# Kernel tuning notes

Measured on AMD Instinct MI355X. Metric: run time of the kernel, lower is better.

## Reference

```python
import jax, jax.numpy as jnp
import numpy as np

B, C, T = 4, 512, 4096


def setup_inputs() -> dict:
    key = jax.random.key(0)
    ks = jax.random.split(key, 9)
    s = 1.0 / np.sqrt(C)
    return {
        "x": jax.random.normal(ks[0], (B, C, T), jnp.float32),
        "Wq": jax.random.normal(ks[1], (C, C), jnp.float32) * s,
        "bq": jax.random.normal(ks[2], (C,), jnp.float32) * 0.01,
        "Wk": jax.random.normal(ks[3], (C, C), jnp.float32) * s,
        "bk": jax.random.normal(ks[4], (C,), jnp.float32) * 0.01,
        "Wv": jax.random.normal(ks[5], (C, C), jnp.float32) * s,
        "bv": jax.random.normal(ks[6], (C,), jnp.float32) * 0.01,
        "Wp": jax.random.normal(ks[7], (C, C), jnp.float32) * s,
        "bp": jax.random.normal(ks[8], (C,), jnp.float32) * 0.01,
    }


def reference(x, Wq, bq, Wk, bk, Wv, bv, Wp, bp):
    # x: [B, C, T]; kernel-size-1 causal convs == pointwise linears over channels.
    b, c, t = x.shape
    q = jnp.einsum('oc,bct->bto', Wq, x) + bq  # [B, T, C]
    k = jnp.einsum('oc,bct->bto', Wk, x) + bk
    v = jnp.einsum('oc,bct->bto', Wv, x) + bv
    scale = jnp.asarray(c, x.dtype) ** -0.5
    w = jnp.einsum('btc,bsc->bts', q, k) * scale  # [B, T, T]
    mask = jnp.tril(jnp.ones((t, t), bool))        # causal: query t attends s<=t
    w = jnp.where(mask, w, -jnp.inf)
    w = jax.nn.softmax(w, axis=-1)
    h = jnp.einsum('bts,bsc->btc', w, v)           # [B, T, C]
    out = jnp.einsum('oc,btc->bot', Wp, h) + bp[None, :, None]  # [B, C, T]
    return x + out
```

## Files before the change

kernel.cpp:

```cpp
#include <hip/hip_runtime.h>

#define NB 4
#define NC 512
#define NT 4096
#define NTILE 528

typedef __attribute__((ext_vector_type(4))) float f32x4;
typedef __attribute__((ext_vector_type(8))) short short8;

typedef const __attribute__((address_space(1))) unsigned int* gp1_t;
typedef __attribute__((address_space(3))) unsigned int* lp3_t;

__device__ __forceinline__ void gload16(const short* g, short* l) {
  __builtin_amdgcn_global_load_lds((gp1_t)g, (lp3_t)l, 16, 0, 0);
}

#define BARRIER() asm volatile("s_barrier" ::: "memory")
#define WAITVM0() asm volatile("s_waitcnt vmcnt(0)" ::: "memory")
#define WAITVM4() asm volatile("s_waitcnt vmcnt(4)" ::: "memory")
#define WAITVM8() asm volatile("s_waitcnt vmcnt(8)" ::: "memory")

__device__ __forceinline__ short f2bf(float f) {
  union { float f; unsigned u; } v; v.f = f;
  unsigned r = v.u + 0x7fffu + ((v.u >> 16) & 1u);
  return (short)(r >> 16);
}
__device__ __forceinline__ float bf2f(short s) {
  union { unsigned u; float f; } v; v.u = ((unsigned)(unsigned short)s) << 16;
  return v.f;
}

__device__ __forceinline__ void gemm_tile(const short* __restrict__ A, int lda,
                                          const short* __restrict__ Bg, int ldb,
                                          int m0, int n0, int ksteps,
                                          f32x4 (&acc)[4][4], short* lds) {
  const int tid  = threadIdx.x;
  const int lane = tid & 63;
  const int wv   = tid >> 6;
  const int wm = (wv >> 1) * 64;
  const int wn = (wv & 1) * 64;
  const int srow = wv * 16 + (lane >> 2);
  const int scol = (lane & 3) * 8;
  const int fm  = lane & 15;
  const int fko = (lane >> 4) * 8;

  const short* Ap0 = A  + (size_t)(m0 + srow) * lda + scol;
  const short* Ap1 = Ap0 + (size_t)64 * lda;
  const short* Bp0 = Bg + (size_t)(n0 + srow) * ldb + scol;
  const short* Bp1 = Bp0 + (size_t)64 * ldb;

  auto issue = [&](int kt) {
    short* base = lds + (kt % 3) * 8192;
    const int k0 = kt * 32;
    gload16(Ap0 + k0, base + wv * 512);
    gload16(Ap1 + k0, base + 2048 + wv * 512);
    gload16(Bp0 + k0, base + 4096 + wv * 512);
    gload16(Bp1 + k0, base + 6144 + wv * 512);
  };

  issue(0);
  if (ksteps > 1) issue(1);
  for (int kt = 0; kt < ksteps; ++kt) {
    const short* As = lds + (kt % 3) * 8192;
    const short* Bs = As + 4096;
    if (kt) BARRIER();
    if (kt + 2 < ksteps)      { issue(kt + 2); WAITVM8(); }
    else if (kt + 1 < ksteps) { WAITVM4(); }
    else                      { WAITVM0(); }
    BARRIER();
    short8 af[4], bfr[4];
#pragma unroll
    for (int i = 0; i < 4; ++i)
      af[i] = *(const short8*)(As + (wm + i * 16 + fm) * 32 + fko);
#pragma unroll
    for (int j = 0; j < 4; ++j)
      bfr[j] = *(const short8*)(Bs + (wn + j * 16 + fm) * 32 + fko);
#pragma unroll
    for (int i = 0; i < 4; ++i)
#pragma unroll
      for (int j = 0; j < 4; ++j)
        acc[i][j] = __builtin_amdgcn_mfma_f32_16x16x32_bf16(af[i], bfr[j], acc[i][j], 0, 0, 0);
  }
}

#define ACC_INIT                                  \
  f32x4 acc[4][4];                                \
  {                                               \
    const f32x4 z = {0.f, 0.f, 0.f, 0.f};         \
    for (int i = 0; i < 4; ++i)                   \
      for (int j = 0; j < 4; ++j) acc[i][j] = z;  \
  }

#define EPI_IDX                                   \
  const int lane = threadIdx.x & 63;              \
  const int wave = threadIdx.x >> 6;              \
  const int wm = (wave >> 1) * 64;                \
  const int wn = (wave & 1) * 64;

#define GEMM_LDS __shared__ short lds[24576];

__device__ __forceinline__ void xcd_rowchunk(int x, int nrows, int& row, int& chunk) {
  const int xcd  = x & 7;
  const int slot = x >> 3;
  row   = nrows - 1 - (xcd + 8 * (slot >> 2));
  chunk = slot & 3;
}

__global__ __launch_bounds__(256) void k_transpose(const float* __restrict__ x,
                                                   short* __restrict__ xT) {
  __shared__ float tile[32][33];
  const int b  = blockIdx.z;
  const int t0 = blockIdx.x * 32;
  const int c0 = blockIdx.y * 32;
  const int tx = threadIdx.x & 31;
  const int ty = threadIdx.x >> 5;
  const float* xp = x + ((size_t)b * NC + c0) * NT + t0;
#pragma unroll
  for (int i = 0; i < 32; i += 8)
    tile[ty + i][tx] = xp[(size_t)(ty + i) * NT + tx];
  __syncthreads();
  short* op = xT + ((size_t)b * NT + t0) * NC + c0;
#pragma unroll
  for (int i = 0; i < 32; i += 8)
    op[(size_t)(ty + i) * NC + tx] = f2bf(tile[tx][ty + i]);
}

__global__ __launch_bounds__(256) void k_wcvt(const float* __restrict__ s0, const float* __restrict__ s1,
                                              const float* __restrict__ s2, const float* __restrict__ s3,
                                              short* __restrict__ d0, short* __restrict__ d1,
                                              short* __restrict__ d2, short* __restrict__ d3) {
  const float* s; short* d;
  switch (blockIdx.y) {
    case 0: s = s0; d = d0; break;
    case 1: s = s1; d = d1; break;
    case 2: s = s2; d = d2; break;
    default: s = s3; d = d3; break;
  }
  const int i = (blockIdx.x * 256 + threadIdx.x) * 4;
  const float4 v = *(const float4*)(s + i);
  short4 o;
  o.x = f2bf(v.x); o.y = f2bf(v.y); o.z = f2bf(v.z); o.w = f2bf(v.w);
  *(short4*)(d + i) = o;
}

__global__ __launch_bounds__(256, 3) void k_qkv(const short* __restrict__ xT,
                                                const short* __restrict__ Wq,
                                                const float* __restrict__ bq,
                                                const short* __restrict__ Wk,
                                                const float* __restrict__ bk,
                                                const short* __restrict__ Wv,
                                                const float* __restrict__ bv,
                                                short* __restrict__ Q,
                                                short* __restrict__ K,
                                                short* __restrict__ VT) {
  GEMM_LDS;
  const int b = blockIdx.z;
  const int y = blockIdx.y;
  int row, chunk;
  xcd_rowchunk((int)blockIdx.x, NT / 128, row, chunk);
  const short* Xb = xT + (size_t)b * NT * NC;
  ACC_INIT;
  if (y < 2) {
    const short* W = (y == 0) ? Wq : Wk;
    const float* bias = (y == 0) ? bq : bk;
    short* O = ((y == 0) ? Q : K) + (size_t)b * NT * NC;
    const int m0 = row * 128;
    const int n0 = chunk * 128;
    gemm_tile(Xb, NC, W, NC, m0, n0, NC / 32, acc, lds);
    EPI_IDX;
#pragma unroll
    for (int j = 0; j < 4; ++j) {
      const int n = n0 + wn + j * 16 + (lane & 15);
      const float bv_ = bias[n];
#pragma unroll
      for (int i = 0; i < 4; ++i) {
        const int mb = m0 + wm + i * 16 + ((lane >> 4) * 4);
#pragma unroll
        for (int r = 0; r < 4; ++r)
          O[(size_t)(mb + r) * NC + n] = f2bf(acc[i][j][r] + bv_);
      }
    }
  } else {
    const int n0 = row * 128;
    const int m0 = chunk * 128;
    gemm_tile(Wv, NC, Xb, NC, m0, n0, NC / 32, acc, lds);
    EPI_IDX;
    short* O = VT + (size_t)b * NC * NT;
#pragma unroll
    for (int j = 0; j < 4; ++j) {
      const int n = n0 + wn + j * 16 + (lane & 15);
#pragma unroll
      for (int i = 0; i < 4; ++i) {
        const int mb = m0 + wm + i * 16 + ((lane >> 4) * 4);
#pragma unroll
        for (int r = 0; r < 4; ++r)
          O[(size_t)(mb + r) * NT + n] = f2bf(acc[i][j][r] + bv[mb + r]);
      }
    }
  }
}

__global__ __launch_bounds__(256, 3) void k_scores(const short* __restrict__ Q,
                                                   const short* __restrict__ K,
                                                   short* __restrict__ P,
                                                   float* __restrict__ Lrow) {
  const int p = (((int)blockIdx.x & 7) * 66) + ((int)blockIdx.x >> 3);
  int bm = 0, bn = 0;
  {
    int base = 0;
    for (int sr = 0; sr < 4; ++sr) {
      bool done = false;
      for (int sc = 0; sc <= sr; ++sc) {
        const int sz = (sc == sr) ? 36 : 64;
        if (p < base + sz) {
          const int q = p - base;
          int i, j;
          if (sc == sr) {
            i = 0;
            while ((i + 1) * (i + 2) / 2 <= q) ++i;
            j = q - i * (i + 1) / 2;
          } else { i = q >> 3; j = q & 7; }
          bm = sr * 8 + i; bn = sc * 8 + j;
          done = true; break;
        }
        base += sz;
      }
      if (done) break;
    }
  }
  GEMM_LDS;
  const int b  = blockIdx.z;
  const int m0 = bm * 128;
  const int n0 = bn * 128;
  ACC_INIT;
  gemm_tile(Q + (size_t)b * NT * NC, NC, K + (size_t)b * NT * NC, NC,
            m0, n0, NC / 32, acc, lds);
  EPI_IDX;
  const float scale = 0.04419417382415922f;
  const int idx = bm * (bm + 1) / 2 + bn;
  short* Tp = P + ((size_t)b * NTILE + (size_t)idx) * 16384;
  float* Lp = Lrow + (size_t)b * NT;
  float psum[4][4];
#pragma unroll
  for (int i = 0; i < 4; ++i)
#pragma unroll
    for (int r = 0; r < 4; ++r) psum[i][r] = 0.f;

  if (bn < bm) {
#pragma unroll
    for (int j = 0; j < 4; ++j) {
      const int ln = wn + j * 16 + (lane & 15);
#pragma unroll
      for (int i = 0; i < 4; ++i) {
        const int lmb = wm + i * 16 + ((lane >> 4) * 4);
#pragma unroll
        for (int r = 0; r < 4; ++r) {
          const short pb = f2bf(__expf(acc[i][j][r] * scale));
          Tp[(lmb + r) * 128 + ln] = pb;
          psum[i][r] += bf2f(pb);
        }
      }
    }
  } else {
#pragma unroll
    for (int j = 0; j < 4; ++j) {
      const int ln = wn + j * 16 + (lane & 15);
      const int n  = n0 + ln;
#pragma unroll
      for (int i = 0; i < 4; ++i) {
        const int lmb = wm + i * 16 + ((lane >> 4) * 4);
#pragma unroll
        for (int r = 0; r < 4; ++r) {
          const int m = m0 + lmb + r;
          float pr = 0.f;
          short pb = 0;
          if (n <= m) {
            pb = f2bf(__expf(acc[i][j][r] * scale));
            pr = bf2f(pb);
          }
          Tp[(lmb + r) * 128 + ln] = pb;
          psum[i][r] += pr;
        }
      }
    }
  }
#pragma unroll
  for (int i = 0; i < 4; ++i)
#pragma unroll
    for (int r = 0; r < 4; ++r) {
      float v = psum[i][r];
      v += __shfl_xor(v, 1);
      v += __shfl_xor(v, 2);
      v += __shfl_xor(v, 4);
      v += __shfl_xor(v, 8);
      if ((lane & 15) == 0) {
        const int m = m0 + wm + i * 16 + ((lane >> 4) * 4) + r;
        atomicAdd(&Lp[m], v);
      }
    }
}

__global__ __launch_bounds__(256, 3) void k_pv(const short* __restrict__ P,
                                               const short* __restrict__ VT,
                                               const float* __restrict__ Lr,
                                               short* __restrict__ H) {
  GEMM_LDS;
  const int b = blockIdx.z;
  int bm, chunk;
  xcd_rowchunk((int)blockIdx.x, NT / 128, bm, chunk);
  const int m0 = bm * 128;
  const int n0 = chunk * 128;
  const int ksteps = (bm + 1) * 4;

  const short* Ptri = P + ((size_t)b * NTILE + (size_t)bm * (bm + 1) / 2) * 16384;
  const short* Bg   = VT + (size_t)b * NC * NT;

  ACC_INIT;
  const int tid  = threadIdx.x;
  const int lane = tid & 63;
  const int wv   = tid >> 6;
  const int wm = (wv >> 1) * 64;
  const int wn = (wv & 1) * 64;
  const int srow = wv * 16 + (lane >> 2);
  const int scol = (lane & 3) * 8;
  const int fm  = lane & 15;
  const int fko = (lane >> 4) * 8;

  const short* Bp0 = Bg + (size_t)(n0 + srow) * NT + scol;
  const short* Bp1 = Bp0 + (size_t)64 * NT;

  auto issue = [&](int kt) {
    short* base = lds + (kt % 3) * 8192;
    const short* At = Ptri + (size_t)(kt >> 2) * 16384 + (kt & 3) * 32;
    const short* Ap0 = At + srow * 128 + scol;
    const int k0 = kt * 32;
    gload16(Ap0, base + wv * 512);
    gload16(Ap0 + 64 * 128, base + 2048 + wv * 512);
    gload16(Bp0 + k0, base + 4096 + wv * 512);
    gload16(Bp1 + k0, base + 6144 + wv * 512);
  };

  issue(0);
  if (ksteps > 1) issue(1);
  for (int kt = 0; kt < ksteps; ++kt) {
    const short* As = lds + (kt % 3) * 8192;
    const short* Bs = As + 4096;
    if (kt) BARRIER();
    if (kt + 2 < ksteps)      { issue(kt + 2); WAITVM8(); }
    else if (kt + 1 < ksteps) { WAITVM4(); }
    else                      { WAITVM0(); }
    BARRIER();
    short8 af[4], bfr[4];
#pragma unroll
    for (int i = 0; i < 4; ++i)
      af[i] = *(const short8*)(As + (wm + i * 16 + fm) * 32 + fko);
#pragma unroll
    for (int j = 0; j < 4; ++j)
      bfr[j] = *(const short8*)(Bs + (wn + j * 16 + fm) * 32 + fko);
#pragma unroll
    for (int i = 0; i < 4; ++i)
#pragma unroll
      for (int j = 0; j < 4; ++j)
        acc[i][j] = __builtin_amdgcn_mfma_f32_16x16x32_bf16(af[i], bfr[j], acc[i][j], 0, 0, 0);
  }

  const float* L = Lr + (size_t)b * NT;
  short* Hp = H + (size_t)b * NT * NC;
#pragma unroll
  for (int i = 0; i < 4; ++i) {
    const int mb = m0 + wm + i * 16 + ((lane >> 4) * 4);
    float rinv[4];
#pragma unroll
    for (int r = 0; r < 4; ++r) rinv[r] = 1.f / L[mb + r];
#pragma unroll
    for (int j = 0; j < 4; ++j) {
      const int n = n0 + wn + j * 16 + (lane & 15);
#pragma unroll
      for (int r = 0; r < 4; ++r)
        Hp[(size_t)(mb + r) * NC + n] = f2bf(acc[i][j][r] * rinv[r]);
    }
  }
}

__global__ __launch_bounds__(256, 3) void k_out(const short* __restrict__ W,
                                                const short* __restrict__ H,
                                                const float* __restrict__ bias,
                                                const float* __restrict__ x,
                                                float* __restrict__ out) {
  GEMM_LDS;
  const int b = blockIdx.z;
  int row, chunk;
  xcd_rowchunk((int)blockIdx.x, NT / 128, row, chunk);
  const int n0 = row * 128;
  const int m0 = chunk * 128;
  ACC_INIT;
  gemm_tile(W, NC, H + (size_t)b * NT * NC, NC, m0, n0, NC / 32, acc, lds);
  EPI_IDX;
#pragma unroll
  for (int j = 0; j < 4; ++j) {
    const int n = n0 + wn + j * 16 + (lane & 15);
#pragma unroll
    for (int i = 0; i < 4; ++i) {
      const int mb = m0 + wm + i * 16 + ((lane >> 4) * 4);
#pragma unroll
      for (int r = 0; r < 4; ++r) {
        const int m = mb + r;
        const size_t idx = ((size_t)b * NC + m) * NT + n;
        out[idx] = acc[i][j][r] + bias[m] + x[idx];
      }
    }
  }
}

extern "C" void kernel_launch(void* const* d_in, const int* in_sizes, int n_in,
                              void* d_out, int out_size, void* d_ws, size_t ws_size,
                              hipStream_t stream) {
  (void)in_sizes; (void)n_in; (void)out_size; (void)ws_size;
  const float* x  = (const float*)d_in[0];
  const float* Wq = (const float*)d_in[1];
  const float* bq = (const float*)d_in[2];
  const float* Wk = (const float*)d_in[3];
  const float* bk = (const float*)d_in[4];
  const float* Wv = (const float*)d_in[5];
  const float* bv = (const float*)d_in[6];
  const float* Wp = (const float*)d_in[7];
  const float* bp = (const float*)d_in[8];
  float* out = (float*)d_out;

  char* ws = (char*)d_ws;
  size_t off = 0;
  auto alloc = [&](size_t bytes) { char* p = ws + off; off += bytes; return p; };
  short* xT  = (short*)alloc((size_t)NB * NT * NC * 2);
  short* Qb  = (short*)alloc((size_t)NB * NT * NC * 2);
  short* Kb  = (short*)alloc((size_t)NB * NT * NC * 2);
  short* VTb = (short*)alloc((size_t)NB * NC * NT * 2);
  short* Hb  = (short*)alloc((size_t)NB * NT * NC * 2);
  short* Wqb = (short*)alloc((size_t)NC * NC * 2);
  short* Wkb = (short*)alloc((size_t)NC * NC * 2);
  short* Wvb = (short*)alloc((size_t)NC * NC * 2);
  short* Wpb = (short*)alloc((size_t)NC * NC * 2);
  float* Lr  = (float*)alloc((size_t)NB * NT * 4);
  short* Pb  = (short*)alloc((size_t)NB * NTILE * 16384 * 2);

  hipMemsetAsync(Lr, 0, (size_t)NB * NT * 4, stream);

  const dim3 blk(256);
  k_wcvt<<<dim3(NC * NC / 1024, 4), blk, 0, stream>>>(Wq, Wk, Wv, Wp, Wqb, Wkb, Wvb, Wpb);

  k_transpose<<<dim3(NT / 32, NC / 32, NB), blk, 0, stream>>>(x, xT);

  k_qkv<<<dim3(128, 3, NB), blk, 0, stream>>>(xT, Wqb, bq, Wkb, bk, Wvb, bv, Qb, Kb, VTb);

  k_scores<<<dim3(NTILE, 1, NB), blk, 0, stream>>>(Qb, Kb, Pb, Lr);
  k_pv<<<dim3(128, 1, NB), blk, 0, stream>>>(Pb, VTb, Lr, Hb);
  k_out<<<dim3(128, 1, NB), blk, 0, stream>>>(Wpb, Hb, bp, x, out);
}
```

Before: 287.8 us.

## Split PV GEMM along K into balanced chunks with atomic fp32 accumulation

The causal P·V kernel is split along the key dimension into segments of at most eight 128-wide tiles. This turns the triangular, badly imbalanced 128-block launch into 320 blocks per batch of bounded work. Partial results go into an fp32 buffer via global atomic adds, and a new kernel then normalises by the row sums and converts to bf16. In exchange it adds a 32 MB memset, atomic traffic to a large fp32 buffer, and an extra conversion pass.

```diff
diff --git a/kernel.cpp b/kernel.cpp
--- a/kernel.cpp
+++ b/kernel.cpp
@@ -13,6 +13,15 @@
 
 __device__ __forceinline__ void gload16(const short* g, short* l) {
   __builtin_amdgcn_global_load_lds((gp1_t)g, (lp3_t)l, 16, 0, 0);
+}
+
+__device__ __forceinline__ void atom_add_f32(float* p, float v) {
+#if __has_builtin(__builtin_amdgcn_global_atomic_fadd_f32)
+  typedef __attribute__((address_space(1))) float gfloat;
+  __builtin_amdgcn_global_atomic_fadd_f32((gfloat*)p, v);
+#else
+  atomicAdd(p, v);
+#endif
 }
 
 #define BARRIER() asm volatile("s_barrier" ::: "memory")
@@ -302,15 +311,28 @@
 
 __global__ __launch_bounds__(256, 3) void k_pv(const short* __restrict__ P,
                                                const short* __restrict__ VT,
-                                               const float* __restrict__ Lr,
-                                               short* __restrict__ H) {
+                                               float* __restrict__ Hacc) {
   GEMM_LDS;
   const int b = blockIdx.z;
-  int bm, chunk;
-  xcd_rowchunk((int)blockIdx.x, NT / 128, bm, chunk);
+  const int x = (int)blockIdx.x;
+  const int xcd  = x & 7;
+  const int slot = x >> 3;
+  const int chunk = slot & 3;
+  const int p = ((slot >> 2) << 3) + xcd;
+  int bm = 31, s = 0;
+  {
+    int accum = 0;
+    for (int r = 31; r >= 0; --r) {
+      const int ns = (r + 8) >> 3;
+      if (p < accum + ns) { bm = r; s = p - accum; break; }
+      accum += ns;
+    }
+  }
+  const int tc = min(8, bm + 1 - s * 8);
+  const int ksteps = tc * 4;
   const int m0 = bm * 128;
   const int n0 = chunk * 128;
-  const int ksteps = (bm + 1) * 4;
+  const int gbase = s * 32;
 
   const short* Ptri = P + ((size_t)b * NTILE + (size_t)bm * (bm + 1) / 2) * 16384;
   const short* Bg   = VT + (size_t)b * NC * NT;
@@ -331,13 +353,13 @@
 
   auto issue = [&](int kt) {
     short* base = lds + (kt % 3) * 8192;
-    const short* At = Ptri + (size_t)(kt >> 2) * 16384 + (kt & 3) * 32;
+    const int g = gbase + kt;
+    const short* At = Ptri + (size_t)(g >> 2) * 16384 + (g & 3) * 32;
     const short* Ap0 = At + srow * 128 + scol;
-    const int k0 = kt * 32;
     gload16(Ap0, base + wv * 512);
     gload16(Ap0 + 64 * 128, base + 2048 + wv * 512);
-    gload16(Bp0 + k0, base + 4096 + wv * 512);
-    gload16(Bp1 + k0, base + 6144 + wv * 512);
+    gload16(Bp0 + g * 32, base + 4096 + wv * 512);
+    gload16(Bp1 + g * 32, base + 6144 + wv * 512);
   };
 
   issue(0);
@@ -364,22 +386,32 @@
         acc[i][j] = __builtin_amdgcn_mfma_f32_16x16x32_bf16(af[i], bfr[j], acc[i][j], 0, 0, 0);
   }
 
-  const float* L = Lr + (size_t)b * NT;
-  short* Hp = H + (size_t)b * NT * NC;
+  float* Ha = Hacc + (size_t)b * NT * NC;
 #pragma unroll
   for (int i = 0; i < 4; ++i) {
     const int mb = m0 + wm + i * 16 + ((lane >> 4) * 4);
-    float rinv[4];
-#pragma unroll
-    for (int r = 0; r < 4; ++r) rinv[r] = 1.f / L[mb + r];
 #pragma unroll
     for (int j = 0; j < 4; ++j) {
       const int n = n0 + wn + j * 16 + (lane & 15);
 #pragma unroll
       for (int r = 0; r < 4; ++r)
-        Hp[(size_t)(mb + r) * NC + n] = f2bf(acc[i][j][r] * rinv[r]);
-    }
-  }
+        atom_add_f32(&Ha[(size_t)(mb + r) * NC + n], acc[i][j][r]);
+    }
+  }
+}
+
+__global__ __launch_bounds__(256) void k_hcvt(const float* __restrict__ Hacc,
+                                              const float* __restrict__ Lr,
+                                              short* __restrict__ H) {
+  const int tid = threadIdx.x;
+  const int row = (int)blockIdx.x * 2 + (tid >> 7);
+  const int col = (tid & 127) * 4;
+  const float rinv = 1.f / Lr[row];
+  const float4 v = *(const float4*)(Hacc + (size_t)row * NC + col);
+  short4 o;
+  o.x = f2bf(v.x * rinv); o.y = f2bf(v.y * rinv);
+  o.z = f2bf(v.z * rinv); o.w = f2bf(v.w * rinv);
+  *(short4*)(H + (size_t)row * NC + col) = o;
 }
 
 __global__ __launch_bounds__(256, 3) void k_out(const short* __restrict__ W,
@@ -435,6 +467,7 @@
   short* Kb  = (short*)alloc((size_t)NB * NT * NC * 2);
   short* VTb = (short*)alloc((size_t)NB * NC * NT * 2);
   short* Hb  = (short*)alloc((size_t)NB * NT * NC * 2);
+  float* Hacc = (float*)alloc((size_t)NB * NT * NC * 4);
   short* Wqb = (short*)alloc((size_t)NC * NC * 2);
   short* Wkb = (short*)alloc((size_t)NC * NC * 2);
   short* Wvb = (short*)alloc((size_t)NC * NC * 2);
@@ -443,6 +476,7 @@
   short* Pb  = (short*)alloc((size_t)NB * NTILE * 16384 * 2);
 
   hipMemsetAsync(Lr, 0, (size_t)NB * NT * 4, stream);
+  hipMemsetAsync(Hacc, 0, (size_t)NB * NT * NC * 4, stream);
 
   const dim3 blk(256);
   k_wcvt<<<dim3(NC * NC / 1024, 4), blk, 0, stream>>>(Wq, Wk, Wv, Wp, Wqb, Wkb, Wvb, Wpb);
@@ -452,6 +486,7 @@
   k_qkv<<<dim3(128, 3, NB), blk, 0, stream>>>(xT, Wqb, bq, Wkb, bk, Wvb, bv, Qb, Kb, VTb);
 
   k_scores<<<dim3(NTILE, 1, NB), blk, 0, stream>>>(Qb, Kb, Pb, Lr);
-  k_pv<<<dim3(128, 1, NB), blk, 0, stream>>>(Pb, VTb, Lr, Hb);
+  k_pv<<<dim3(320, 1, NB), blk, 0, stream>>>(Pb, VTb, Hacc);
+  k_hcvt<<<dim3(NB * NT / 2), blk, 0, stream>>>(Hacc, Lr, Hb);
   k_out<<<dim3(128, 1, NB), blk, 0, stream>>>(Wpb, Hb, bp, x, out);
 }
```

Measured after the change: 315.3 us. +9.6%, slower.
